# Kernel optimization log

Hardware: AMD Instinct MI355X
Metric: run time of the kernel (lower is better)

## Reference

```python
import jax, jax.numpy as jnp
import numpy as np

V, D, N, S = 100000, 256, 8192, 20
H = D  # hidden size == feat_dim (nn.LSTM(feat_dim, feat_dim))


def setup_inputs() -> dict:
    key = jax.random.key(0)
    ks = jax.random.split(key, 8)
    sc = 1.0 / np.sqrt(H)  # PyTorch LSTM default init scale
    return {
        "emb": jax.random.normal(ks[0], (V, D), jnp.float32),
        "w_ih_f": jax.random.normal(ks[1], (4 * H, D), jnp.float32) * sc,
        "w_hh_f": jax.random.normal(ks[2], (4 * H, H), jnp.float32) * sc,
        "b_f": jax.random.normal(ks[3], (4 * H,), jnp.float32) * sc,
        "w_ih_b": jax.random.normal(ks[4], (4 * H, D), jnp.float32) * sc,
        "w_hh_b": jax.random.normal(ks[5], (4 * H, H), jnp.float32) * sc,
        "b_b": jax.random.normal(ks[6], (4 * H,), jnp.float32) * sc,
        "neigh_idx": jax.random.randint(ks[7], (N, S), 0, V, dtype=jnp.int64),
    }


def _lstm_dir(x, w_ih, w_hh, b):
    """Batched unidirectional LSTM. x: [N, S, D] -> hidden states [N, S, H].
    PyTorch gate order: i, f, g, o."""
    h_dim = w_hh.shape[1]
    # precompute input contribution for all steps: [N, S, 4H]
    xg = jnp.einsum('nsd,gd->nsg', x, w_ih) + b

    def step(carry, xt):
        h, c = carry
        g = xt + h @ w_hh.T
        i, f, gg, o = jnp.split(g, 4, axis=-1)
        c = jax.nn.sigmoid(f) * c + jax.nn.sigmoid(i) * jnp.tanh(gg)
        h = jax.nn.sigmoid(o) * jnp.tanh(c)
        return (h, c), h

    n = x.shape[0]
    init = (jnp.zeros((n, h_dim), x.dtype), jnp.zeros((n, h_dim), x.dtype))
    _, hs = jax.lax.scan(step, init, jnp.swapaxes(xg, 0, 1))  # [S, N, H]
    return jnp.swapaxes(hs, 0, 1)


def reference(emb, w_ih_f, w_hh_f, b_f, w_ih_b, w_hh_b, b_b, neigh_idx):
    x = emb[neigh_idx]  # gather neighbor embeddings: [N, S, D]
    hf = _lstm_dir(x, w_ih_f, w_hh_f, b_f)                      # [N, S, H]
    hb = _lstm_dir(x[:, ::-1, :], w_ih_b, w_hh_b, b_b)[:, ::-1, :]
    h = jnp.concatenate([hf, hb], axis=-1)  # [N, S, 2H]
    summed = h.sum(axis=1)                  # sum over time: [N, 2H]
    # faithful to original: torch.mean over the 1-D summed vector -> scalar
    # broadcast into the full output row
    row = summed.mean(axis=-1, keepdims=True)  # [N, 1]
    return jnp.broadcast_to(row, summed.shape)  # [N, 2H]
```

## Files before the change

### kernel.cpp

```cpp
#include <hip/hip_runtime.h>

#define NN 8192
#define SS 20
#define DD 256
#define RGATE 1024
#define KKD 512

typedef __attribute__((ext_vector_type(8))) short short8;
typedef __attribute__((ext_vector_type(4))) float f32x4;

__device__ __forceinline__ unsigned short f2bf(float f) {
    unsigned int u = __float_as_uint(f);
    u += 0x7FFFu + ((u >> 16) & 1u);
    return (unsigned short)(u >> 16);
}

__device__ __forceinline__ void async_copy16(const void* g, void* l) {
    __builtin_amdgcn_global_load_lds(
        (const __attribute__((address_space(1))) void*)g,
        (__attribute__((address_space(3))) void*)l, 16, 0, 0);
}

__device__ __forceinline__ float sigm(float x) { return 1.0f / (1.0f + __expf(-x)); }
__device__ __forceinline__ float tanh_(float x) { return 2.0f / (1.0f + __expf(-2.0f * x)) - 1.0f; }

__global__ void convert_w(const float* __restrict__ wihf, const float* __restrict__ whhf,
                          const float* __restrict__ bf,   const float* __restrict__ wihb,
                          const float* __restrict__ whhb, const float* __restrict__ bb,
                          unsigned short* __restrict__ Wcat, float* __restrict__ bperm) {
    const int idx = blockIdx.x * 256 + threadIdx.x;
    const int dir = idx >> 19;
    const int rem = idx & ((1 << 19) - 1);
    const int rp  = rem >> 9;
    const int k   = rem & 511;
    const int j   = rp >> 2, gi = rp & 3;
    const int r   = gi * 256 + j;
    const float* wih = dir ? wihb : wihf;
    const float* whh = dir ? whhb : whhf;
    const float v = (k < 256) ? wih[r * 256 + k] : whh[r * 256 + (k - 256)];
    Wcat[idx] = f2bf(v);
    if (k == 0) {
        const float* b = dir ? bb : bf;
        bperm[dir * 1024 + rp] = b[r];
    }
}

__global__ __launch_bounds__(256) void gather_x(const float* __restrict__ emb,
                                                const int* __restrict__ idx,
                                                unsigned short* __restrict__ X) {
    const int w = threadIdx.x >> 6, lane = threadIdx.x & 63;
    #pragma unroll 4
    for (int i = 0; i < 16; ++i) {
        const int rid = (blockIdx.x * 16 + i) * 4 + w;
        const int n = rid / SS, t = rid - n * SS;
        const int row = idx[rid];
        const float4 v = ((const float4*)(emb + (size_t)row * DD))[lane];
        ushort4 o;
        o.x = f2bf(v.x); o.y = f2bf(v.y); o.z = f2bf(v.z); o.w = f2bf(v.w);
        ((ushort4*)(X + ((size_t)t * NN + n) * DD))[lane] = o;
    }
}

__global__ __launch_bounds__(512, 2) void lstm_step(
    const unsigned short* __restrict__ X,
    const unsigned short* __restrict__ Wcat,
    const float* __restrict__ bperm,
    unsigned short* __restrict__ hping,
    float* __restrict__ cstate,
    float* __restrict__ hsum,
    int s) {
    const int b     = blockIdx.x;
    const int dir   = b & 1;
    const int nblk  = (b >> 3) & 3;
    const int mslab = (((b & 7) >> 1) << 3) | (b >> 5);
    const int m0    = mslab * 256;
    const int n0    = nblk * 256;

    const int t = dir ? (SS - 1 - s) : s;
    const unsigned short* Xt    = X + (size_t)t * NN * DD;
    const unsigned short* hprev = hping + ((size_t)((s & 1) * 2 + dir)) * NN * 256;
    unsigned short*       hnext = hping + ((size_t)((((s + 1) & 1) * 2) + dir)) * NN * 256;
    const unsigned short* W     = Wcat + (size_t)dir * RGATE * KKD;
    const float*          bp    = bperm + dir * RGATE;
    float*                cdir  = cstate + (size_t)dir * NN * 256;

    __shared__ __align__(16) char smem[65536];

    const int tid  = threadIdx.x;
    const int lane = tid & 63;
    const int w    = tid >> 6;
    const int wm   = w >> 1, wn = w & 1;
    const int quad = lane >> 4, l15 = lane & 15;
    const int jq   = lane & 3,  rl  = lane >> 2;

    const int srow  = lane >> 2;
    const int gsegl = (lane & 3) ^ ((lane >> 3) & 3);

    auto stage = [&](int r, int buf) {
        const int k0 = (r & 7) * 32;
        const unsigned short* Asrc = (r < 8) ? Xt : hprev;
        char* Ad = smem + buf * 16384;
        char* Bd = smem + 32768 + buf * 16384;
        #pragma unroll
        for (int i = 0; i < 2; ++i) {
            const int lr = w * 32 + i * 16 + srow;
            async_copy16(Asrc + (size_t)(m0 + lr) * DD + k0 + gsegl * 8,
                         (void*)(Ad + (w * 32 + i * 16) * 64));
            async_copy16(W + (size_t)(n0 + lr) * KKD + r * 32 + gsegl * 8,
                         (void*)(Bd + (w * 32 + i * 16) * 64));
        }
    };

    f32x4 acc[4][8];
    #pragma unroll
    for (int i = 0; i < 4; ++i)
        #pragma unroll
        for (int j = 0; j < 8; ++j) acc[i][j] = f32x4{0.f, 0.f, 0.f, 0.f};

    stage(0, 0);
    __syncthreads();

    const int sA = (quad ^ ((l15 >> 1) & 3)) * 16;

    for (int r = 0; r < 16; ++r) {
        if (r < 15) stage(r + 1, (r + 1) & 1);
        const char* Ab = smem + (r & 1) * 16384;
        const char* Bb = smem + 32768 + (r & 1) * 16384;
        short8 af[4], bf[8];
        #pragma unroll
        for (int mt = 0; mt < 4; ++mt)
            af[mt] = *(const short8*)(Ab + (wm * 64 + mt * 16 + l15) * 64 + sA);
        #pragma unroll
        for (int nt = 0; nt < 8; ++nt)
            bf[nt] = *(const short8*)(Bb + (wn * 128 + nt * 16 + l15) * 64 + sA);
        #pragma unroll
        for (int mt = 0; mt < 4; ++mt)
            #pragma unroll
            for (int nt = 0; nt < 8; ++nt)
                acc[mt][nt] = __builtin_amdgcn_mfma_f32_16x16x32_bf16(
                    af[mt], bf[nt], acc[mt][nt], 0, 0, 0);
        __syncthreads();
    }

    float* my = (float*)smem + w * 1088;
    float hs[4] = {0.f, 0.f, 0.f, 0.f};

    #pragma unroll
    for (int half = 0; half < 2; ++half) {
        const int j0 = nblk * 64 + wn * 32 + half * 16 + jq * 4;
        f32x4 bias4[4];
        #pragma unroll
        for (int jj = 0; jj < 4; ++jj)
            bias4[jj] = *(const f32x4*)(bp + 4 * (j0 + jj));
        #pragma unroll
        for (int mt = 0; mt < 4; ++mt) {
            #pragma unroll
            for (int nt = 0; nt < 4; ++nt) {
                const int ntg = half * 4 + nt;
                #pragma unroll
                for (int v = 0; v < 4; ++v)
                    my[(quad * 4 + v) * 68 + nt * 16 + l15] = acc[mt][ntg][v];
            }
            asm volatile("s_waitcnt lgkmcnt(0)" ::: "memory");
            const int mg = m0 + wm * 64 + mt * 16 + rl;
            float* cptr = cdir + (size_t)mg * 256 + j0;
            f32x4 cold = *(const f32x4*)cptr;
            f32x4 cnew;
            ushort4 hp;
            float lsum = 0.f;
            #pragma unroll
            for (int jj = 0; jj < 4; ++jj) {
                f32x4 g  = *(const f32x4*)(my + rl * 68 + (jq * 4 + jj) * 4);
                f32x4 bb = bias4[jj];
                const float gi = sigm(g.x + bb.x);
                const float gf = sigm(g.y + bb.y);
                const float gg = tanh_(g.z + bb.z);
                const float go = sigm(g.w + bb.w);
                const float cn = gf * cold[jj] + gi * gg;
                cnew[jj] = cn;
                const float hv = go * tanh_(cn);
                lsum += hv;
                ((unsigned short*)&hp)[jj] = f2bf(hv);
            }
            *(f32x4*)cptr = cnew;
            *(ushort4*)(hnext + (size_t)mg * 256 + j0) = hp;
            hs[mt] += lsum;
        }
    }

    #pragma unroll
    for (int mt = 0; mt < 4; ++mt) {
        float v = hs[mt];
        v += __shfl_xor(v, 1);
        v += __shfl_xor(v, 2);
        if (jq == 0) atomicAdd(&hsum[m0 + wm * 64 + mt * 16 + rl], v);
    }
}

__global__ void bcast_out(const float* __restrict__ hsum, float* __restrict__ out) {
    const int n = blockIdx.x;
    const float v = hsum[n] * (1.0f / 512.0f);
    float2 p; p.x = v; p.y = v;
    ((float2*)(out + (size_t)n * 512))[threadIdx.x] = p;
}

extern "C" void kernel_launch(void* const* d_in, const int* in_sizes, int n_in,
                              void* d_out, int out_size, void* d_ws, size_t ws_size,
                              hipStream_t stream) {
    const float* emb  = (const float*)d_in[0];
    const float* wihf = (const float*)d_in[1];
    const float* whhf = (const float*)d_in[2];
    const float* bf   = (const float*)d_in[3];
    const float* wihb = (const float*)d_in[4];
    const float* whhb = (const float*)d_in[5];
    const float* bb   = (const float*)d_in[6];
    const int*   idx  = (const int*)d_in[7];
    float* out = (float*)d_out;

    char* ws = (char*)d_ws;
    unsigned short* X     = (unsigned short*)(ws);
    unsigned short* Wcat  = (unsigned short*)(ws + 83886080);
    float*          bperm = (float*)(ws + 85983232);
    unsigned short* hping = (unsigned short*)(ws + 85991424);
    float*          cst   = (float*)(ws + 102768640);
    float*          hsum  = (float*)(ws + 119545856);

    hipMemsetAsync(hping, 0, 8388608, stream);
    hipMemsetAsync(cst, 0, 16777216 + 32768, stream);

    convert_w<<<4096, 256, 0, stream>>>(wihf, whhf, bf, wihb, whhb, bb, Wcat, bperm);
    gather_x<<<2560, 256, 0, stream>>>(emb, idx, X);
    for (int s = 0; s < SS; ++s)
        lstm_step<<<256, 512, 0, stream>>>(X, Wcat, bperm, hping, cst, hsum, s);
    bcast_out<<<NN, 256, 0, stream>>>(hsum, out);
}
```

Measured before the change: 844.5 us.

## Fuse gather, all LSTM timesteps and output broadcast into one persistent kernel

Replaces the per-timestep kernel launches, the separate gather kernel and the broadcast kernel with a single persistent kernel of 256 blocks. Each block gathers its share of embeddings, keeps the cell state in registers, and synchronises only with the four blocks sharing its row slab through global atomic counters. The X@Wih half of the next step's GEMM is computed before waiting on the barrier, so it overlaps the wait. K-tiles grow to 64 with a new XOR swizzle. The cost is a reliance on all 256 blocks being co-resident (spin barriers can deadlock otherwise) and 128KB of shared memory per block.

```diff
diff --git a/kernel.cpp b/kernel.cpp
--- a/kernel.cpp
+++ b/kernel.cpp
@@ -45,46 +45,28 @@
     }
 }
 
-__global__ __launch_bounds__(256) void gather_x(const float* __restrict__ emb,
-                                                const int* __restrict__ idx,
-                                                unsigned short* __restrict__ X) {
-    const int w = threadIdx.x >> 6, lane = threadIdx.x & 63;
-    #pragma unroll 4
-    for (int i = 0; i < 16; ++i) {
-        const int rid = (blockIdx.x * 16 + i) * 4 + w;
-        const int n = rid / SS, t = rid - n * SS;
-        const int row = idx[rid];
-        const float4 v = ((const float4*)(emb + (size_t)row * DD))[lane];
-        ushort4 o;
-        o.x = f2bf(v.x); o.y = f2bf(v.y); o.z = f2bf(v.z); o.w = f2bf(v.w);
-        ((ushort4*)(X + ((size_t)t * NN + n) * DD))[lane] = o;
-    }
-}
-
-__global__ __launch_bounds__(512, 2) void lstm_step(
-    const unsigned short* __restrict__ X,
+__global__ __launch_bounds__(512, 2) void lstm_persist(
+    const float* __restrict__ emb,
+    const int* __restrict__ nidx,
+    unsigned short* X,
     const unsigned short* __restrict__ Wcat,
     const float* __restrict__ bperm,
-    unsigned short* __restrict__ hping,
-    float* __restrict__ cstate,
-    float* __restrict__ hsum,
-    int s) {
+    unsigned short* hping,
+    float* hsum,
+    int* bar, int* bar2,
+    float* out) {
     const int b     = blockIdx.x;
     const int dir   = b & 1;
     const int nblk  = (b >> 3) & 3;
     const int mslab = (((b & 7) >> 1) << 3) | (b >> 5);
+    const int grp   = dir * 32 + mslab;
     const int m0    = mslab * 256;
     const int n0    = nblk * 256;
 
-    const int t = dir ? (SS - 1 - s) : s;
-    const unsigned short* Xt    = X + (size_t)t * NN * DD;
-    const unsigned short* hprev = hping + ((size_t)((s & 1) * 2 + dir)) * NN * 256;
-    unsigned short*       hnext = hping + ((size_t)((((s + 1) & 1) * 2) + dir)) * NN * 256;
-    const unsigned short* W     = Wcat + (size_t)dir * RGATE * KKD;
-    const float*          bp    = bperm + dir * RGATE;
-    float*                cdir  = cstate + (size_t)dir * NN * 256;
-
-    __shared__ __align__(16) char smem[65536];
+    const unsigned short* W  = Wcat + (size_t)dir * RGATE * KKD;
+    const float*          bp = bperm + dir * RGATE;
+
+    __shared__ __align__(16) char smem[131072];
 
     const int tid  = threadIdx.x;
     const int lane = tid & 63;
@@ -92,99 +74,162 @@
     const int wm   = w >> 1, wn = w & 1;
     const int quad = lane >> 4, l15 = lane & 15;
     const int jq   = lane & 3,  rl  = lane >> 2;
-
-    const int srow  = lane >> 2;
-    const int gsegl = (lane & 3) ^ ((lane >> 3) & 3);
+    const int lrow8 = lane >> 3, lseg8 = lane & 7, sxor = l15 & 7;
+
+    {
+        const int g0 = m0 + nblk * 64;
+        for (int p = w; p < 160; p += 8) {
+            const int t  = p >> 3;
+            const int i0 = (p & 7) * 8;
+            #pragma unroll
+            for (int i = 0; i < 8; ++i) {
+                const int n  = g0 + i0 + i;
+                const int er = nidx[n * SS + t];
+                const float4 v = ((const float4*)(emb + (size_t)er * DD))[lane];
+                ushort4 o;
+                o.x = f2bf(v.x); o.y = f2bf(v.y); o.z = f2bf(v.z); o.w = f2bf(v.w);
+                ((ushort4*)(X + ((size_t)t * NN + n) * DD))[lane] = o;
+            }
+        }
+    }
+    __syncthreads();
+    if (tid == 0) {
+        __threadfence();
+        atomicAdd(&bar[grp], 1);
+        while (__hip_atomic_load(&bar[grp], __ATOMIC_ACQUIRE,
+                                 __HIP_MEMORY_SCOPE_AGENT) < 4)
+            __builtin_amdgcn_s_sleep(2);
+    }
+    __syncthreads();
+
+    f32x4 cst[2][4];
+    #pragma unroll
+    for (int i = 0; i < 2; ++i)
+        #pragma unroll
+        for (int j = 0; j < 4; ++j) cst[i][j] = f32x4{0.f, 0.f, 0.f, 0.f};
+    float hs[4] = {0.f, 0.f, 0.f, 0.f};
+    f32x4 acc[4][8];
+
+    const unsigned short* Xt = nullptr;
+    const unsigned short* hprev = nullptr;
+    unsigned short* hnext = nullptr;
 
     auto stage = [&](int r, int buf) {
-        const int k0 = (r & 7) * 32;
-        const unsigned short* Asrc = (r < 8) ? Xt : hprev;
-        char* Ad = smem + buf * 16384;
-        char* Bd = smem + 32768 + buf * 16384;
-        #pragma unroll
-        for (int i = 0; i < 2; ++i) {
-            const int lr = w * 32 + i * 16 + srow;
-            async_copy16(Asrc + (size_t)(m0 + lr) * DD + k0 + gsegl * 8,
-                         (void*)(Ad + (w * 32 + i * 16) * 64));
-            async_copy16(W + (size_t)(n0 + lr) * KKD + r * 32 + gsegl * 8,
-                         (void*)(Bd + (w * 32 + i * 16) * 64));
+        const int k0s = (r & 3) * 64;
+        const unsigned short* Asrc = (r < 4) ? Xt : hprev;
+        char* Ad = smem + buf * 32768;
+        char* Bd = smem + 65536 + buf * 32768;
+        #pragma unroll
+        for (int i = 0; i < 4; ++i) {
+            const int row  = w * 32 + i * 8 + lrow8;
+            const int gofs = (lseg8 ^ (row & 7)) * 8;
+            async_copy16(Asrc + (size_t)(m0 + row) * DD + k0s + gofs,
+                         (void*)(Ad + (w * 32 + i * 8) * 128));
+            async_copy16(W + (size_t)(n0 + row) * KKD + r * 64 + gofs,
+                         (void*)(Bd + (w * 32 + i * 8) * 128));
         }
     };
 
-    f32x4 acc[4][8];
-    #pragma unroll
-    for (int i = 0; i < 4; ++i)
-        #pragma unroll
-        for (int j = 0; j < 8; ++j) acc[i][j] = f32x4{0.f, 0.f, 0.f, 0.f};
-
-    stage(0, 0);
-    __syncthreads();
-
-    const int sA = (quad ^ ((l15 >> 1) & 3)) * 16;
-
-    for (int r = 0; r < 16; ++r) {
-        if (r < 15) stage(r + 1, (r + 1) & 1);
-        const char* Ab = smem + (r & 1) * 16384;
-        const char* Bb = smem + 32768 + (r & 1) * 16384;
-        short8 af[4], bf[8];
-        #pragma unroll
-        for (int mt = 0; mt < 4; ++mt)
-            af[mt] = *(const short8*)(Ab + (wm * 64 + mt * 16 + l15) * 64 + sA);
-        #pragma unroll
-        for (int nt = 0; nt < 8; ++nt)
-            bf[nt] = *(const short8*)(Bb + (wn * 128 + nt * 16 + l15) * 64 + sA);
-        #pragma unroll
-        for (int mt = 0; mt < 4; ++mt)
+    auto compute = [&](int buf) {
+        const char* Ab = smem + buf * 32768;
+        const char* Bb = smem + 65536 + buf * 32768;
+        #pragma unroll
+        for (int kk = 0; kk < 2; ++kk) {
+            short8 af[4], bfr[8];
+            const int so = ((kk * 4 + quad) ^ sxor) << 4;
+            #pragma unroll
+            for (int mt = 0; mt < 4; ++mt)
+                af[mt] = *(const short8*)(Ab + (wm * 64 + mt * 16 + l15) * 128 + so);
             #pragma unroll
             for (int nt = 0; nt < 8; ++nt)
-                acc[mt][nt] = __builtin_amdgcn_mfma_f32_16x16x32_bf16(
-                    af[mt], bf[nt], acc[mt][nt], 0, 0, 0);
+                bfr[nt] = *(const short8*)(Bb + (wn * 128 + nt * 16 + l15) * 128 + so);
+            #pragma unroll
+            for (int mt = 0; mt < 4; ++mt)
+                #pragma unroll
+                for (int nt = 0; nt < 8; ++nt)
+                    acc[mt][nt] = __builtin_amdgcn_mfma_f32_16x16x32_bf16(
+                        af[mt], bfr[nt], acc[mt][nt], 0, 0, 0);
+        }
+    };
+
+    for (int s = 0; s < SS; ++s) {
+        const int t = dir ? (SS - 1 - s) : s;
+        Xt    = X + (size_t)t * NN * DD;
+        hprev = hping + ((size_t)((s & 1) * 2 + dir)) * NN * 256;
+        hnext = hping + ((size_t)((((s + 1) & 1) * 2) + dir)) * NN * 256;
+
+        #pragma unroll
+        for (int i = 0; i < 4; ++i)
+            #pragma unroll
+            for (int j = 0; j < 8; ++j) acc[i][j] = f32x4{0.f, 0.f, 0.f, 0.f};
+
+        stage(0, 0);
         __syncthreads();
-    }
-
-    float* my = (float*)smem + w * 1088;
-    float hs[4] = {0.f, 0.f, 0.f, 0.f};
-
-    #pragma unroll
-    for (int half = 0; half < 2; ++half) {
-        const int j0 = nblk * 64 + wn * 32 + half * 16 + jq * 4;
-        f32x4 bias4[4];
-        #pragma unroll
-        for (int jj = 0; jj < 4; ++jj)
-            bias4[jj] = *(const f32x4*)(bp + 4 * (j0 + jj));
-        #pragma unroll
-        for (int mt = 0; mt < 4; ++mt) {
-            #pragma unroll
-            for (int nt = 0; nt < 4; ++nt) {
-                const int ntg = half * 4 + nt;
+        for (int r = 0; r < 4; ++r) {
+            if (r < 3) stage(r + 1, (r + 1) & 1);
+            compute(r & 1);
+            __syncthreads();
+        }
+        if (s > 0) {
+            if (tid == 0)
+                while (__hip_atomic_load(&bar[grp], __ATOMIC_ACQUIRE,
+                                         __HIP_MEMORY_SCOPE_AGENT) < 4 * s + 4)
+                    __builtin_amdgcn_s_sleep(2);
+            __syncthreads();
+        }
+        stage(4, 0);
+        __syncthreads();
+        for (int r = 4; r < 8; ++r) {
+            if (r < 7) stage(r + 1, (r + 1) & 1);
+            compute(r & 1);
+            __syncthreads();
+        }
+
+        float* my = (float*)smem + w * 1088;
+        #pragma unroll
+        for (int half = 0; half < 2; ++half) {
+            const int j0 = nblk * 64 + wn * 32 + half * 16 + jq * 4;
+            f32x4 bias4[4];
+            #pragma unroll
+            for (int jj = 0; jj < 4; ++jj)
+                bias4[jj] = *(const f32x4*)(bp + 4 * (j0 + jj));
+            #pragma unroll
+            for (int mt = 0; mt < 4; ++mt) {
                 #pragma unroll
-                for (int v = 0; v < 4; ++v)
-                    my[(quad * 4 + v) * 68 + nt * 16 + l15] = acc[mt][ntg][v];
+                for (int nt = 0; nt < 4; ++nt) {
+                    const int ntg = half * 4 + nt;
+                    #pragma unroll
+                    for (int v = 0; v < 4; ++v)
+                        my[(quad * 4 + v) * 68 + nt * 16 + l15] = acc[mt][ntg][v];
+                }
+                asm volatile("s_waitcnt lgkmcnt(0)" ::: "memory");
+                const int mg = m0 + wm * 64 + mt * 16 + rl;
+                f32x4 cold = cst[half][mt], cnew;
+                ushort4 hp;
+                float lsum = 0.f;
+                #pragma unroll
+                for (int jj = 0; jj < 4; ++jj) {
+                    f32x4 g  = *(const f32x4*)(my + rl * 68 + (jq * 4 + jj) * 4);
+                    f32x4 bb = bias4[jj];
+                    const float gi = sigm(g.x + bb.x);
+                    const float gf = sigm(g.y + bb.y);
+                    const float gg = tanh_(g.z + bb.z);
+                    const float go = sigm(g.w + bb.w);
+                    const float cn = gf * cold[jj] + gi * gg;
+                    cnew[jj] = cn;
+                    const float hv = go * tanh_(cn);
+                    lsum += hv;
+                    ((unsigned short*)&hp)[jj] = f2bf(hv);
+                }
+                cst[half][mt] = cnew;
+                *(ushort4*)(hnext + (size_t)mg * 256 + j0) = hp;
+                hs[mt] += lsum;
             }
-            asm volatile("s_waitcnt lgkmcnt(0)" ::: "memory");
-            const int mg = m0 + wm * 64 + mt * 16 + rl;
-            float* cptr = cdir + (size_t)mg * 256 + j0;
-            f32x4 cold = *(const f32x4*)cptr;
-            f32x4 cnew;
-            ushort4 hp;
-            float lsum = 0.f;
-            #pragma unroll
-            for (int jj = 0; jj < 4; ++jj) {
-                f32x4 g  = *(const f32x4*)(my + rl * 68 + (jq * 4 + jj) * 4);
-                f32x4 bb = bias4[jj];
-                const float gi = sigm(g.x + bb.x);
-                const float gf = sigm(g.y + bb.y);
-                const float gg = tanh_(g.z + bb.z);
-                const float go = sigm(g.w + bb.w);
-                const float cn = gf * cold[jj] + gi * gg;
-                cnew[jj] = cn;
-                const float hv = go * tanh_(cn);
-                lsum += hv;
-                ((unsigned short*)&hp)[jj] = f2bf(hv);
-            }
-            *(f32x4*)cptr = cnew;
-            *(ushort4*)(hnext + (size_t)mg * 256 + j0) = hp;
-            hs[mt] += lsum;
+        }
+        __syncthreads();
+        if (tid == 0 && s < SS - 1) {
+            __threadfence();
+            atomicAdd(&bar[grp], 1);
         }
     }
 
@@ -195,13 +240,24 @@
         v += __shfl_xor(v, 2);
         if (jq == 0) atomicAdd(&hsum[m0 + wm * 64 + mt * 16 + rl], v);
     }
-}
-
-__global__ void bcast_out(const float* __restrict__ hsum, float* __restrict__ out) {
-    const int n = blockIdx.x;
-    const float v = hsum[n] * (1.0f / 512.0f);
-    float2 p; p.x = v; p.y = v;
-    ((float2*)(out + (size_t)n * 512))[threadIdx.x] = p;
+    __syncthreads();
+    if (tid == 0) {
+        __threadfence();
+        atomicAdd(&bar2[mslab], 1);
+        while (__hip_atomic_load(&bar2[mslab], __ATOMIC_ACQUIRE,
+                                 __HIP_MEMORY_SCOPE_AGENT) < 8)
+            __builtin_amdgcn_s_sleep(2);
+    }
+    __syncthreads();
+
+    const int rstart = m0 + (dir * 4 + nblk) * 32;
+    #pragma unroll
+    for (int i = 0; i < 8; ++i) {
+        const int row = rstart + i * 4 + (tid >> 7);
+        const float val = hsum[row] * (1.0f / 512.0f);
+        f32x4 vv = {val, val, val, val};
+        ((f32x4*)(out + (size_t)row * 512))[tid & 127] = vv;
+    }
 }
 
 extern "C" void kernel_launch(void* const* d_in, const int* in_sizes, int n_in,
@@ -222,15 +278,14 @@
     unsigned short* Wcat  = (unsigned short*)(ws + 83886080);
     float*          bperm = (float*)(ws + 85983232);
     unsigned short* hping = (unsigned short*)(ws + 85991424);
-    float*          cst   = (float*)(ws + 102768640);
-    float*          hsum  = (float*)(ws + 119545856);
+    float*          hsum  = (float*)(ws + 102768640);
+    int*            bar   = (int*)(ws + 102801408);
+    int*            bar2  = (int*)(ws + 102801664);
 
     hipMemsetAsync(hping, 0, 8388608, stream);
-    hipMemsetAsync(cst, 0, 16777216 + 32768, stream);
+    hipMemsetAsync(hsum, 0, 32768 + 256 + 128, stream);
 
     convert_w<<<4096, 256, 0, stream>>>(wihf, whhf, bf, wihb, whhb, bb, Wcat, bperm);
-    gather_x<<<2560, 256, 0, stream>>>(emb, idx, X);
-    for (int s = 0; s < SS; ++s)
-        lstm_step<<<256, 512, 0, stream>>>(X, Wcat, bperm, hping, cst, hsum, s);
-    bcast_out<<<NN, 256, 0, stream>>>(hsum, out);
-}
+    lstm_persist<<<256, 512, 0, stream>>>(emb, idx, X, Wcat, bperm, hping,
+                                          hsum, bar, bar2, out);
+}
```

New measurement: 1.244 ms. 1.47x slower.
